# Optimization experiments

Measured on AMD Instinct MI355X. Metric: run time of the kernel, lower is better.

The kernel has to match this reference:

```python
import jax, jax.numpy as jnp
import numpy as np

B, T, C, H = 2, 2048, 1024, 16
HD = C // H  # head dim = 64


def setup_inputs() -> dict:
    key = jax.random.key(0)
    ks = jax.random.split(key, 9)
    s = 1.0 / np.sqrt(C)
    return {
        "x": jax.random.normal(ks[0], (B, T, C), dtype=jnp.float32),
        "Wq": jax.random.normal(ks[1], (C, C), dtype=jnp.float32) * s,
        "bq": jax.random.normal(ks[2], (C,), dtype=jnp.float32) * 0.02,
        "Wk": jax.random.normal(ks[3], (C, C), dtype=jnp.float32) * s,
        "bk": jax.random.normal(ks[4], (C,), dtype=jnp.float32) * 0.02,
        "Wv": jax.random.normal(ks[5], (C, C), dtype=jnp.float32) * s,
        "bv": jax.random.normal(ks[6], (C,), dtype=jnp.float32) * 0.02,
        "Wo": jax.random.normal(ks[7], (C, C), dtype=jnp.float32) * s,
        "bo": jax.random.normal(ks[8], (C,), dtype=jnp.float32) * 0.02,
    }


def reference(x, Wq, bq, Wk, bk, Wv, bv, Wo, bo):
    # Projections (torch Linear: x @ W.T + b; here W stored pre-transposed as [C_in, C_out])
    q = x @ Wq + bq  # (B,T,C)
    k = x @ Wk + bk
    v = x @ Wv + bv
    # Split heads: (B,T,C) -> (B,H,T,HD)
    q = q.reshape(B, T, H, HD).transpose(0, 2, 1, 3)
    k = k.reshape(B, T, H, HD).transpose(0, 2, 1, 3)
    v = v.reshape(B, T, H, HD).transpose(0, 2, 1, 3)
    # NOTE: original module never applies a causal mask despite its name.
    score = jnp.einsum("bhqd,bhkd->bhqk", q, k) / jnp.sqrt(jnp.float32(HD))
    score = jax.nn.softmax(score, axis=-1)
    y = jnp.einsum("bhqk,bhkd->bhqd", score, v)
    y = y.transpose(0, 2, 1, 3).reshape(B, T, C)
    # dropout is identity in eval mode
    return y @ Wo + bo
```

## Files before the change

kernel.cpp:

```cpp
#include <hip/hip_runtime.h>
#include <math.h>

#define B_ 2
#define T_ 2048
#define C_ 1024
#define H_ 16
#define HD_ 64
#define M_ (B_*T_)

typedef _Float16 half4v __attribute__((ext_vector_type(4)));
typedef _Float16 half8v __attribute__((ext_vector_type(8)));
typedef float f32x4 __attribute__((ext_vector_type(4)));

__global__ __launch_bounds__(256) void cast_f16_kernel(
    const float* __restrict__ src, _Float16* __restrict__ dst, int n4)
{
  int i = blockIdx.x * 256 + threadIdx.x;
  if (i < n4) {
    float4 v = ((const float4*)src)[i];
    half4v h; h[0] = (_Float16)v.x; h[1] = (_Float16)v.y;
    h[2] = (_Float16)v.z; h[3] = (_Float16)v.w;
    ((half4v*)dst)[i] = h;
  }
}

__global__ __launch_bounds__(256) void transpose_cast_kernel(
    const float* __restrict__ W, _Float16* __restrict__ Wt)
{
  __shared__ float tile[32][33];
  const int tx = threadIdx.x, ty = threadIdx.y;
  const int n0 = blockIdx.x * 32, k0 = blockIdx.y * 32;
#pragma unroll
  for (int r = 0; r < 4; r++) {
    int k = ty + r * 8;
    tile[k][tx] = W[(size_t)(k0 + k) * C_ + n0 + tx];
  }
  __syncthreads();
#pragma unroll
  for (int r = 0; r < 4; r++) {
    int n = ty + r * 8;
    Wt[(size_t)(n0 + n) * C_ + k0 + tx] = (_Float16)tile[tx][n];
  }
}

__global__ __launch_bounds__(256) void concat_bias_kernel(
    const float* __restrict__ bq, const float* __restrict__ bk,
    const float* __restrict__ bv, float* __restrict__ b3)
{
  int i = blockIdx.x * 256 + threadIdx.x;
  const float* s = (i < 1024) ? bq : ((i < 2048) ? bk : bv);
  b3[i] = s[i & 1023];
}

template <int BM, int BN, int EPI>
__global__ __launch_bounds__(256) void gemm_f16_kernel(
    const _Float16* __restrict__ A, const _Float16* __restrict__ Bw,
    const float* __restrict__ bias,
    _Float16* __restrict__ o0, _Float16* __restrict__ o1,
    _Float16* __restrict__ o2, float* __restrict__ of)
{
  constexpr int FM = BM / 32, FN = BN / 32;
  __shared__ __align__(16) _Float16 smem[(BM + BN) * 32];
  _Float16* As = smem;
  _Float16* Bs = smem + BM * 32;
  const int t = threadIdx.x;
  const int w = t >> 6, lane = t & 63, l15 = lane & 15, quad = lane >> 4;
  const int wm = (w & 1) * (BM / 2), wn = (w >> 1) * (BN / 2);
  const int bm = blockIdx.y * BM, bn = blockIdx.x * BN;

  f32x4 acc[FM][FN];
#pragma unroll
  for (int i = 0; i < FM; i++)
#pragma unroll
    for (int j = 0; j < FN; j++) acc[i][j] = (f32x4){0.f, 0.f, 0.f, 0.f};

  for (int k0 = 0; k0 < 1024; k0 += 32) {
#pragma unroll
    for (int i = 0; i < BM * 4 / 256; i++) {
      int slot = t + i * 256;
      int row = slot >> 2, cp = slot & 3;
      int c = cp ^ ((row >> 1) & 3);
      *(uint4*)((char*)As + slot * 16) =
          *(const uint4*)(A + (size_t)(bm + row) * 1024 + k0 + c * 8);
    }
#pragma unroll
    for (int i = 0; i < BN * 4 / 256; i++) {
      int slot = t + i * 256;
      int row = slot >> 2, cp = slot & 3;
      int c = cp ^ ((row >> 1) & 3);
      *(uint4*)((char*)Bs + slot * 16) =
          *(const uint4*)(Bw + (size_t)(bn + row) * 1024 + k0 + c * 8);
    }
    __syncthreads();

    half8v af[FM], bf[FN];
#pragma unroll
    for (int mt = 0; mt < FM; mt++) {
      int row = wm + mt * 16 + l15;
      int ch = quad ^ ((row >> 1) & 3);
      af[mt] = *(const half8v*)((char*)As + row * 64 + ch * 16);
    }
#pragma unroll
    for (int nt = 0; nt < FN; nt++) {
      int row = wn + nt * 16 + l15;
      int ch = quad ^ ((row >> 1) & 3);
      bf[nt] = *(const half8v*)((char*)Bs + row * 64 + ch * 16);
    }
#pragma unroll
    for (int mt = 0; mt < FM; mt++)
#pragma unroll
      for (int nt = 0; nt < FN; nt++)
        acc[mt][nt] = __builtin_amdgcn_mfma_f32_16x16x32_f16(
            af[mt], bf[nt], acc[mt][nt], 0, 0, 0);
    __syncthreads();
  }

#pragma unroll
  for (int mt = 0; mt < FM; mt++)
#pragma unroll
    for (int nt = 0; nt < FN; nt++) {
      int n = bn + wn + nt * 16 + l15;
      float bv = bias[n];
#pragma unroll
      for (int r = 0; r < 4; r++) {
        int m = bm + wm + mt * 16 + quad * 4 + r;
        float v = acc[mt][nt][r] + bv;
        if (EPI == 0) {
          if (bn < 1024) {
            o0[(size_t)m * 1024 + n] = (_Float16)(v * 0.125f);
          } else if (bn < 2048) {
            o1[(size_t)m * 1024 + (n - 1024)] = (_Float16)v;
          } else {
            int dg = n - 2048;
            int hh = dg >> 6, hd = dg & 63;
            int bb = m >> 11, tt = m & 2047;
            o2[(((size_t)(bb * H_ + hh)) * 64 + hd) * 2048 + tt] = (_Float16)v;
          }
        } else {
          of[(size_t)m * 1024 + n] = v;
        }
      }
    }
}

__global__ __launch_bounds__(256) void attn_f16_kernel(
    const _Float16* __restrict__ Qh, const _Float16* __restrict__ Kh,
    const _Float16* __restrict__ Vt, _Float16* __restrict__ Yh)
{
  __shared__ __align__(16) _Float16 Ks[64 * 64];
  __shared__ __align__(16) _Float16 Vs[64 * 64];
  const int t = threadIdx.x;
  const int w = t >> 6, lane = t & 63, l15 = lane & 15, quad = lane >> 4;
  const int qt = blockIdx.x, h = blockIdx.y, b = blockIdx.z;
  const int qg = qt * 64 + w * 16 + l15;
  const size_t qoff = ((size_t)(b * T_ + qg)) * C_ + h * HD_;

  half8v qf[2];
  qf[0] = *(const half8v*)(Qh + qoff + quad * 8);
  qf[1] = *(const half8v*)(Qh + qoff + 32 + quad * 8);

  f32x4 o[4];
#pragma unroll
  for (int i = 0; i < 4; i++) o[i] = (f32x4){0.f, 0.f, 0.f, 0.f};
  float m_run = -INFINITY, l_run = 0.f;

  const size_t kbase = ((size_t)b * T_) * C_ + h * HD_;
  const size_t vbase = ((size_t)(b * H_ + h)) * HD_ * 2048;

  for (int kt0 = 0; kt0 < T_; kt0 += 64) {
#pragma unroll
    for (int i = 0; i < 2; i++) {
      int slot = t + i * 256;
      int row = slot >> 3, cp = slot & 7;
      int c = cp ^ (row & 7);
      *(uint4*)((char*)Ks + slot * 16) =
          *(const uint4*)(Kh + kbase + (size_t)(kt0 + row) * C_ + c * 8);
      *(uint4*)((char*)Vs + slot * 16) =
          *(const uint4*)(Vt + vbase + (size_t)row * 2048 + kt0 + c * 8);
    }
    __syncthreads();

    f32x4 s[4];
#pragma unroll
    for (int kt = 0; kt < 4; kt++) {
      s[kt] = (f32x4){0.f, 0.f, 0.f, 0.f};
      int key = kt * 16 + l15;
#pragma unroll
      for (int ks = 0; ks < 2; ks++) {
        half8v kf = *(const half8v*)(
            (char*)Ks + key * 128 + (((ks * 4 + quad) ^ (key & 7)) * 16));
        s[kt] = __builtin_amdgcn_mfma_f32_16x16x32_f16(kf, qf[ks], s[kt], 0, 0, 0);
      }
    }

    float tmax = -INFINITY;
#pragma unroll
    for (int kt = 0; kt < 4; kt++)
#pragma unroll
      for (int r = 0; r < 4; r++) tmax = fmaxf(tmax, s[kt][r]);
    tmax = fmaxf(tmax, __shfl_xor(tmax, 16));
    tmax = fmaxf(tmax, __shfl_xor(tmax, 32));
    float mnew = fmaxf(m_run, tmax);
    float alpha = __expf(m_run - mnew);

    float psum = 0.f;
    half4v pf[4];
#pragma unroll
    for (int kt = 0; kt < 4; kt++)
#pragma unroll
      for (int r = 0; r < 4; r++) {
        float p = __expf(s[kt][r] - mnew);
        psum += p;
        pf[kt][r] = (_Float16)p;
      }
    psum += __shfl_xor(psum, 16);
    psum += __shfl_xor(psum, 32);
    l_run = l_run * alpha + psum;
    m_run = mnew;
#pragma unroll
    for (int dt = 0; dt < 4; dt++) o[dt] *= alpha;

#pragma unroll
    for (int dt = 0; dt < 4; dt++) {
      int d = dt * 16 + l15;
#pragma unroll
      for (int kt = 0; kt < 4; kt++) {
        half4v vf = *(const half4v*)(
            (char*)Vs + d * 128 + (((kt * 2 + (quad >> 1)) ^ (d & 7)) * 16) +
            (quad & 1) * 8);
        o[dt] = __builtin_amdgcn_mfma_f32_16x16x16f16(vf, pf[kt], o[dt], 0, 0, 0);
      }
    }
    __syncthreads();
  }

  float inv = 1.0f / l_run;
#pragma unroll
  for (int dt = 0; dt < 4; dt++) {
    half4v yv;
#pragma unroll
    for (int r = 0; r < 4; r++) yv[r] = (_Float16)(o[dt][r] * inv);
    *(half4v*)(Yh + qoff + dt * 16 + quad * 4) = yv;
  }
}

extern "C" void kernel_launch(void* const* d_in, const int* in_sizes, int n_in,
                              void* d_out, int out_size, void* d_ws, size_t ws_size,
                              hipStream_t stream) {
  const float* x  = (const float*)d_in[0];
  const float* Wq = (const float*)d_in[1];
  const float* bq = (const float*)d_in[2];
  const float* Wk = (const float*)d_in[3];
  const float* bk = (const float*)d_in[4];
  const float* Wv = (const float*)d_in[5];
  const float* bv = (const float*)d_in[6];
  const float* Wo = (const float*)d_in[7];
  const float* bo = (const float*)d_in[8];
  float* out = (float*)d_out;

  char* ws = (char*)d_ws;
  _Float16* xh   = (_Float16*)(ws);
  _Float16* Qh   = (_Float16*)(ws + (((size_t)8)  << 20));
  _Float16* Kh   = (_Float16*)(ws + (((size_t)16) << 20));
  _Float16* Vt   = (_Float16*)(ws + (((size_t)24) << 20));
  _Float16* Yh   = (_Float16*)(ws + (((size_t)32) << 20));
  _Float16* Wt3  = (_Float16*)(ws + (((size_t)40) << 20));
  _Float16* Wot  = (_Float16*)(ws + (((size_t)46) << 20));
  float*    b3   = (float*)   (ws + (((size_t)48) << 20));

  cast_f16_kernel<<<(M_ * C_ / 4 + 255) / 256, 256, 0, stream>>>(x, xh, M_ * C_ / 4);

  dim3 tg(32, 32), tb(32, 8);
  transpose_cast_kernel<<<tg, tb, 0, stream>>>(Wq, Wt3);
  transpose_cast_kernel<<<tg, tb, 0, stream>>>(Wk, Wt3 + (size_t)1024 * 1024);
  transpose_cast_kernel<<<tg, tb, 0, stream>>>(Wv, Wt3 + (size_t)2048 * 1024);
  transpose_cast_kernel<<<tg, tb, 0, stream>>>(Wo, Wot);
  concat_bias_kernel<<<12, 256, 0, stream>>>(bq, bk, bv, b3);

  gemm_f16_kernel<128, 128, 0><<<dim3(24, 32), 256, 0, stream>>>(
      xh, Wt3, b3, Qh, Kh, Vt, nullptr);

  attn_f16_kernel<<<dim3(T_ / 64, H_, B_), 256, 0, stream>>>(Qh, Kh, Vt, Yh);

  gemm_f16_kernel<64, 128, 1><<<dim3(8, 64), 256, 0, stream>>>(
      Yh, Wot, bo, nullptr, nullptr, nullptr, out);
}
```

Measured before the change: 236.5 us.

## Use direct global-to-LDS loads in GEMM, padded attention LDS, exp2 softmax, merged transposes

The GEMM now stages A/B tiles with global_load_lds (direct global-to-LDS DMA) in place of register round-trips. This drops the XOR swizzle, so LDS fragment reads may see bank conflicts. Attention swaps the XOR swizzle for padded rows (136-byte stride) and computes exponentials with exp2, with log2(e) folded into the Q scale. Probabilities are packed with cvt_pkrtz. The four weight transpose launches are merged into one launch using a z-indexed grid.

```diff
diff --git a/kernel.cpp b/kernel.cpp
--- a/kernel.cpp
+++ b/kernel.cpp
@@ -8,9 +8,15 @@
 #define HD_ 64
 #define M_ (B_*T_)
 
+typedef _Float16 half2v __attribute__((ext_vector_type(2)));
 typedef _Float16 half4v __attribute__((ext_vector_type(4)));
 typedef _Float16 half8v __attribute__((ext_vector_type(8)));
 typedef float f32x4 __attribute__((ext_vector_type(4)));
+
+#define GLD_LDS(gp, lp) \
+  __builtin_amdgcn_global_load_lds( \
+      (const __attribute__((address_space(1))) void*)(gp), \
+      (__attribute__((address_space(3))) void*)(lp), 16, 0, 0)
 
 __global__ __launch_bounds__(256) void cast_f16_kernel(
     const float* __restrict__ src, _Float16* __restrict__ dst, int n4)
@@ -24,9 +30,18 @@
   }
 }
 
-__global__ __launch_bounds__(256) void transpose_cast_kernel(
-    const float* __restrict__ W, _Float16* __restrict__ Wt)
-{
+__global__ __launch_bounds__(256) void transpose_cast_all_kernel(
+    const float* __restrict__ Wq, const float* __restrict__ Wk,
+    const float* __restrict__ Wv, const float* __restrict__ Wo,
+    _Float16* __restrict__ Wt3, _Float16* __restrict__ Wot)
+{
+  const float* W; _Float16* Wt;
+  switch (blockIdx.z) {
+    case 0:  W = Wq; Wt = Wt3; break;
+    case 1:  W = Wk; Wt = Wt3 + (size_t)1024 * 1024; break;
+    case 2:  W = Wv; Wt = Wt3 + (size_t)2048 * 1024; break;
+    default: W = Wo; Wt = Wot; break;
+  }
   __shared__ float tile[32][33];
   const int tx = threadIdx.x, ty = threadIdx.y;
   const int n0 = blockIdx.x * 32, k0 = blockIdx.y * 32;
@@ -60,13 +75,13 @@
     _Float16* __restrict__ o2, float* __restrict__ of)
 {
   constexpr int FM = BM / 32, FN = BN / 32;
-  __shared__ __align__(16) _Float16 smem[(BM + BN) * 32];
-  _Float16* As = smem;
-  _Float16* Bs = smem + BM * 32;
+  __shared__ __align__(16) _Float16 As[BM * 32];
+  __shared__ __align__(16) _Float16 Bs[BN * 32];
   const int t = threadIdx.x;
   const int w = t >> 6, lane = t & 63, l15 = lane & 15, quad = lane >> 4;
   const int wm = (w & 1) * (BM / 2), wn = (w >> 1) * (BN / 2);
   const int bm = blockIdx.y * BM, bn = blockIdx.x * BN;
+  const int lrow = lane >> 2, lcol = (lane & 3) * 8;
 
   f32x4 acc[FM][FN];
 #pragma unroll
@@ -76,36 +91,26 @@
 
   for (int k0 = 0; k0 < 1024; k0 += 32) {
 #pragma unroll
-    for (int i = 0; i < BM * 4 / 256; i++) {
-      int slot = t + i * 256;
-      int row = slot >> 2, cp = slot & 3;
-      int c = cp ^ ((row >> 1) & 3);
-      *(uint4*)((char*)As + slot * 16) =
-          *(const uint4*)(A + (size_t)(bm + row) * 1024 + k0 + c * 8);
-    }
-#pragma unroll
-    for (int i = 0; i < BN * 4 / 256; i++) {
-      int slot = t + i * 256;
-      int row = slot >> 2, cp = slot & 3;
-      int c = cp ^ ((row >> 1) & 3);
-      *(uint4*)((char*)Bs + slot * 16) =
-          *(const uint4*)(Bw + (size_t)(bn + row) * 1024 + k0 + c * 8);
+    for (int i = 0; i < BM / 64; i++) {
+      int ca = w + 4 * i;
+      int row = ca * 16 + lrow;
+      GLD_LDS(A + (size_t)(bm + row) * 1024 + k0 + lcol, As + ca * 512);
+    }
+#pragma unroll
+    for (int i = 0; i < BN / 64; i++) {
+      int cb = w + 4 * i;
+      int row = cb * 16 + lrow;
+      GLD_LDS(Bw + (size_t)(bn + row) * 1024 + k0 + lcol, Bs + cb * 512);
     }
     __syncthreads();
 
     half8v af[FM], bf[FN];
 #pragma unroll
-    for (int mt = 0; mt < FM; mt++) {
-      int row = wm + mt * 16 + l15;
-      int ch = quad ^ ((row >> 1) & 3);
-      af[mt] = *(const half8v*)((char*)As + row * 64 + ch * 16);
-    }
-#pragma unroll
-    for (int nt = 0; nt < FN; nt++) {
-      int row = wn + nt * 16 + l15;
-      int ch = quad ^ ((row >> 1) & 3);
-      bf[nt] = *(const half8v*)((char*)Bs + row * 64 + ch * 16);
-    }
+    for (int mt = 0; mt < FM; mt++)
+      af[mt] = *(const half8v*)(As + (wm + mt * 16 + l15) * 32 + quad * 8);
+#pragma unroll
+    for (int nt = 0; nt < FN; nt++)
+      bf[nt] = *(const half8v*)(Bs + (wn + nt * 16 + l15) * 32 + quad * 8);
 #pragma unroll
     for (int mt = 0; mt < FM; mt++)
 #pragma unroll
@@ -127,7 +132,7 @@
         float v = acc[mt][nt][r] + bv;
         if (EPI == 0) {
           if (bn < 1024) {
-            o0[(size_t)m * 1024 + n] = (_Float16)(v * 0.125f);
+            o0[(size_t)m * 1024 + n] = (_Float16)(v * 0.180336884f);
           } else if (bn < 2048) {
             o1[(size_t)m * 1024 + (n - 1024)] = (_Float16)v;
           } else {
@@ -147,8 +152,8 @@
     const _Float16* __restrict__ Qh, const _Float16* __restrict__ Kh,
     const _Float16* __restrict__ Vt, _Float16* __restrict__ Yh)
 {
-  __shared__ __align__(16) _Float16 Ks[64 * 64];
-  __shared__ __align__(16) _Float16 Vs[64 * 64];
+  __shared__ __align__(16) _Float16 Ks[64 * 68];
+  __shared__ __align__(16) _Float16 Vs[64 * 68];
   const int t = threadIdx.x;
   const int w = t >> 6, lane = t & 63, l15 = lane & 15, quad = lane >> 4;
   const int qt = blockIdx.x, h = blockIdx.y, b = blockIdx.z;
@@ -167,16 +172,16 @@
   const size_t kbase = ((size_t)b * T_) * C_ + h * HD_;
   const size_t vbase = ((size_t)(b * H_ + h)) * HD_ * 2048;
 
+  const int srow = t >> 3, scp = t & 7;
+
   for (int kt0 = 0; kt0 < T_; kt0 += 64) {
 #pragma unroll
     for (int i = 0; i < 2; i++) {
-      int slot = t + i * 256;
-      int row = slot >> 3, cp = slot & 7;
-      int c = cp ^ (row & 7);
-      *(uint4*)((char*)Ks + slot * 16) =
-          *(const uint4*)(Kh + kbase + (size_t)(kt0 + row) * C_ + c * 8);
-      *(uint4*)((char*)Vs + slot * 16) =
-          *(const uint4*)(Vt + vbase + (size_t)row * 2048 + kt0 + c * 8);
+      int row = srow + i * 32;
+      *(uint4*)((char*)Ks + row * 136 + scp * 16) =
+          *(const uint4*)(Kh + kbase + (size_t)(kt0 + row) * C_ + scp * 8);
+      *(uint4*)((char*)Vs + row * 136 + scp * 16) =
+          *(const uint4*)(Vt + vbase + (size_t)row * 2048 + kt0 + scp * 8);
     }
     __syncthreads();
 
@@ -187,8 +192,7 @@
       int key = kt * 16 + l15;
 #pragma unroll
       for (int ks = 0; ks < 2; ks++) {
-        half8v kf = *(const half8v*)(
-            (char*)Ks + key * 128 + (((ks * 4 + quad) ^ (key & 7)) * 16));
+        half8v kf = *(const half8v*)((char*)Ks + key * 136 + (ks * 4 + quad) * 16);
         s[kt] = __builtin_amdgcn_mfma_f32_16x16x32_f16(kf, qf[ks], s[kt], 0, 0, 0);
       }
     }
@@ -201,18 +205,21 @@
     tmax = fmaxf(tmax, __shfl_xor(tmax, 16));
     tmax = fmaxf(tmax, __shfl_xor(tmax, 32));
     float mnew = fmaxf(m_run, tmax);
-    float alpha = __expf(m_run - mnew);
+    float alpha = __builtin_amdgcn_exp2f(m_run - mnew);
 
     float psum = 0.f;
     half4v pf[4];
 #pragma unroll
-    for (int kt = 0; kt < 4; kt++)
-#pragma unroll
-      for (int r = 0; r < 4; r++) {
-        float p = __expf(s[kt][r] - mnew);
-        psum += p;
-        pf[kt][r] = (_Float16)p;
-      }
+    for (int kt = 0; kt < 4; kt++) {
+      float p0 = __builtin_amdgcn_exp2f(s[kt][0] - mnew);
+      float p1 = __builtin_amdgcn_exp2f(s[kt][1] - mnew);
+      float p2 = __builtin_amdgcn_exp2f(s[kt][2] - mnew);
+      float p3 = __builtin_amdgcn_exp2f(s[kt][3] - mnew);
+      psum += (p0 + p1) + (p2 + p3);
+      half2v pk01 = __builtin_bit_cast(half2v, __builtin_amdgcn_cvt_pkrtz(p0, p1));
+      half2v pk23 = __builtin_bit_cast(half2v, __builtin_amdgcn_cvt_pkrtz(p2, p3));
+      pf[kt] = __builtin_shufflevector(pk01, pk23, 0, 1, 2, 3);
+    }
     psum += __shfl_xor(psum, 16);
     psum += __shfl_xor(psum, 32);
     l_run = l_run * alpha + psum;
@@ -225,9 +232,7 @@
       int d = dt * 16 + l15;
 #pragma unroll
       for (int kt = 0; kt < 4; kt++) {
-        half4v vf = *(const half4v*)(
-            (char*)Vs + d * 128 + (((kt * 2 + (quad >> 1)) ^ (d & 7)) * 16) +
-            (quad & 1) * 8);
+        half4v vf = *(const half4v*)((char*)Vs + d * 136 + kt * 32 + quad * 8);
         o[dt] = __builtin_amdgcn_mfma_f32_16x16x16f16(vf, pf[kt], o[dt], 0, 0, 0);
       }
     }
@@ -269,12 +274,8 @@
   float*    b3   = (float*)   (ws + (((size_t)48) << 20));
 
   cast_f16_kernel<<<(M_ * C_ / 4 + 255) / 256, 256, 0, stream>>>(x, xh, M_ * C_ / 4);
-
-  dim3 tg(32, 32), tb(32, 8);
-  transpose_cast_kernel<<<tg, tb, 0, stream>>>(Wq, Wt3);
-  transpose_cast_kernel<<<tg, tb, 0, stream>>>(Wk, Wt3 + (size_t)1024 * 1024);
-  transpose_cast_kernel<<<tg, tb, 0, stream>>>(Wv, Wt3 + (size_t)2048 * 1024);
-  transpose_cast_kernel<<<tg, tb, 0, stream>>>(Wo, Wot);
+  transpose_cast_all_kernel<<<dim3(32, 32, 4), dim3(32, 8), 0, stream>>>(
+      Wq, Wk, Wv, Wo, Wt3, Wot);
   concat_bias_kernel<<<12, 256, 0, stream>>>(bq, bk, bv, b3);
 
   gemm_f16_kernel<128, 128, 0><<<dim3(24, 32), 256, 0, stream>>>(
```

Result: faster. 223.1 us (-5.7%).
